# Kernel optimization log

Measured on AMD Instinct MI355X. Metric: run time of the kernel, lower is better.

Reference implementation:

```python
import jax, jax.numpy as jnp
import numpy as np

B, E, L = 262144, 16, 224  # pixels, endmembers, spectral bands


def setup_inputs() -> dict:
    key = jax.random.key(0)
    kx, ke, kb = jax.random.split(key, 3)
    x = jax.random.uniform(kx, (B, E), dtype=jnp.float32)          # abundances
    endmembers = jax.random.uniform(ke, (E, L), dtype=jnp.float32)  # spectral signatures
    b_s = jax.random.normal(kb, (B,), dtype=jnp.float32) * 0.1      # per-pixel PPNM coeff
    return {"x": x, "endmembers": endmembers, "b_s": b_s}


def reference(x, endmembers, b_s):
    # mat = x @ W : [B, L]
    mat = jnp.matmul(x, endmembers)
    # Original: mat + transpose(matmul(transpose(mat*mat), diag(b_s)))
    # which is exactly a row-wise scale of mat^2 by b_s.
    return mat + b_s[:, None] * (mat * mat)
```

## Files before the change

kernel.cpp:

```cpp
#include <hip/hip_runtime.h>


#define LBANDS 224
#define EMEMB  16
#define GROUPS 56
#define PROWS  4
#define NTHREADS (GROUPS * PROWS)

__global__ __launch_bounds__(NTHREADS) void ppnm_kernel(
    const float* __restrict__ x,
    const float* __restrict__ w,
    const float* __restrict__ bs,
    float* __restrict__ out,
    int B)
{
    const int t  = threadIdx.x;
    const int g  = t % GROUPS;
    const int pr = t / GROUPS;

    float4 Wf[EMEMB];
    #pragma unroll
    for (int k = 0; k < EMEMB; ++k) {
        Wf[k] = *reinterpret_cast<const float4*>(w + k * LBANDS + 4 * g);
    }

    const int tiles = B / PROWS;
    for (int tile = blockIdx.x; tile < tiles; tile += gridDim.x) {
        const int p = tile * PROWS + pr;

        const float b = bs[p];

        const float4* xr = reinterpret_cast<const float4*>(x + p * EMEMB);
        const float4 xa = xr[0];
        const float4 xb = xr[1];
        const float4 xc = xr[2];
        const float4 xd = xr[3];
        float xv[EMEMB] = { xa.x, xa.y, xa.z, xa.w,
                            xb.x, xb.y, xb.z, xb.w,
                            xc.x, xc.y, xc.z, xc.w,
                            xd.x, xd.y, xd.z, xd.w };

        float4 acc = make_float4(0.f, 0.f, 0.f, 0.f);
        #pragma unroll
        for (int k = 0; k < EMEMB; ++k) {
            acc.x = fmaf(xv[k], Wf[k].x, acc.x);
            acc.y = fmaf(xv[k], Wf[k].y, acc.y);
            acc.z = fmaf(xv[k], Wf[k].z, acc.z);
            acc.w = fmaf(xv[k], Wf[k].w, acc.w);
        }

        float4 r;
        r.x = fmaf(b * acc.x, acc.x, acc.x);
        r.y = fmaf(b * acc.y, acc.y, acc.y);
        r.z = fmaf(b * acc.z, acc.z, acc.z);
        r.w = fmaf(b * acc.w, acc.w, acc.w);

        *reinterpret_cast<float4*>(out + p * LBANDS + 4 * g) = r;
    }
}

extern "C" void kernel_launch(void* const* d_in, const int* in_sizes, int n_in,
                              void* d_out, int out_size, void* d_ws, size_t ws_size,
                              hipStream_t stream) {
    const float* x  = (const float*)d_in[0];
    const float* w  = (const float*)d_in[1];
    const float* bs = (const float*)d_in[2];
    float* out = (float*)d_out;

    const int B = in_sizes[2];

    const int grid = 2048;
    ppnm_kernel<<<grid, NTHREADS, 0, stream>>>(x, w, bs, out, B);
}
```

Measured before the change: 299.5 us.

## Software-prefetch next tile's abundances and double rows per block

```diff
diff --git a/kernel.cpp b/kernel.cpp
--- a/kernel.cpp
+++ b/kernel.cpp
@@ -4,10 +4,10 @@
 #define LBANDS 224
 #define EMEMB  16
 #define GROUPS 56
-#define PROWS  4
+#define PROWS  8
 #define NTHREADS (GROUPS * PROWS)
 
-__global__ __launch_bounds__(NTHREADS) void ppnm_kernel(
+__global__ __launch_bounds__(NTHREADS, 4) void ppnm_kernel(
     const float* __restrict__ x,
     const float* __restrict__ w,
     const float* __restrict__ bs,
@@ -25,37 +25,50 @@
     }
 
     const int tiles = B / PROWS;
-    for (int tile = blockIdx.x; tile < tiles; tile += gridDim.x) {
-        const int p = tile * PROWS + pr;
+    int tile = blockIdx.x;
+    if (tile >= tiles) return;
 
-        const float b = bs[p];
+    int p = tile * PROWS + pr;
+    const float4* xr = reinterpret_cast<const float4*>(x + p * EMEMB);
+    float4 xa = xr[0], xb = xr[1], xc = xr[2], xd = xr[3];
+    float  b  = bs[p];
 
-        const float4* xr = reinterpret_cast<const float4*>(x + p * EMEMB);
-        const float4 xa = xr[0];
-        const float4 xb = xr[1];
-        const float4 xc = xr[2];
-        const float4 xd = xr[3];
-        float xv[EMEMB] = { xa.x, xa.y, xa.z, xa.w,
-                            xb.x, xb.y, xb.z, xb.w,
-                            xc.x, xc.y, xc.z, xc.w,
-                            xd.x, xd.y, xd.z, xd.w };
+    for (;;) {
+        const int curp = p;
+        const float4 ca = xa, cb = xb, cc = xc, cd = xd;
+        const float  cbv = b;
 
+        const int next = tile + gridDim.x;
+        if (next < tiles) {
+            p  = next * PROWS + pr;
+            const float4* nr = reinterpret_cast<const float4*>(x + p * EMEMB);
+            xa = nr[0]; xb = nr[1]; xc = nr[2]; xd = nr[3];
+            b  = bs[p];
+        }
+
+        const float xs[EMEMB] = { ca.x, ca.y, ca.z, ca.w,
+                                  cb.x, cb.y, cb.z, cb.w,
+                                  cc.x, cc.y, cc.z, cc.w,
+                                  cd.x, cd.y, cd.z, cd.w };
         float4 acc = make_float4(0.f, 0.f, 0.f, 0.f);
         #pragma unroll
         for (int k = 0; k < EMEMB; ++k) {
-            acc.x = fmaf(xv[k], Wf[k].x, acc.x);
-            acc.y = fmaf(xv[k], Wf[k].y, acc.y);
-            acc.z = fmaf(xv[k], Wf[k].z, acc.z);
-            acc.w = fmaf(xv[k], Wf[k].w, acc.w);
+            acc.x = fmaf(xs[k], Wf[k].x, acc.x);
+            acc.y = fmaf(xs[k], Wf[k].y, acc.y);
+            acc.z = fmaf(xs[k], Wf[k].z, acc.z);
+            acc.w = fmaf(xs[k], Wf[k].w, acc.w);
         }
 
         float4 r;
-        r.x = fmaf(b * acc.x, acc.x, acc.x);
-        r.y = fmaf(b * acc.y, acc.y, acc.y);
-        r.z = fmaf(b * acc.z, acc.z, acc.z);
-        r.w = fmaf(b * acc.w, acc.w, acc.w);
+        r.x = fmaf(cbv * acc.x, acc.x, acc.x);
+        r.y = fmaf(cbv * acc.y, acc.y, acc.y);
+        r.z = fmaf(cbv * acc.z, acc.z, acc.z);
+        r.w = fmaf(cbv * acc.w, acc.w, acc.w);
 
-        *reinterpret_cast<float4*>(out + p * LBANDS + 4 * g) = r;
+        *reinterpret_cast<float4*>(out + curp * LBANDS + 4 * g) = r;
+
+        if (next >= tiles) break;
+        tile = next;
     }
 }
 
```

Result: no change. 295.4 us (-1.4%).
